# Kernel optimization log

Hardware: AMD Instinct MI355X
Metric: run time of the kernel (lower is better)

Reference implementation:

```python
import jax, jax.numpy as jnp
import numpy as np

N_ENTITY = 500000
N_RELATION = 1000
EMB = 128
BATCH = 131072


def setup_inputs() -> dict:
    key = jax.random.key(0)
    k_h, k_r, k_t, k_e, k_rel = jax.random.split(key, 5)
    head = jax.random.randint(k_h, (BATCH,), 0, N_ENTITY)
    rel = jax.random.randint(k_r, (BATCH,), 0, N_RELATION)
    tail = jax.random.randint(k_t, (BATCH,), 0, N_ENTITY)
    triple = jnp.stack([head, rel, tail], axis=1)  # [B,3] int
    # init_weights: uniform(-0.1, 0.1) for embeddings
    entity_emb = jax.random.uniform(k_e, (N_ENTITY, EMB), jnp.float32, -0.1, 0.1)
    relation_emb = jax.random.uniform(k_rel, (N_RELATION, EMB), jnp.float32, -0.1, 0.1)
    De = jnp.eye(EMB, dtype=jnp.float32)
    Dr = jnp.eye(EMB, dtype=jnp.float32)
    b_c = jnp.zeros((BATCH, EMB), dtype=jnp.float32)
    return {"triple": triple, "entity_emb": entity_emb, "relation_emb": relation_emb,
            "De": De, "Dr": Dr, "b_c": b_c}


def reference(triple, entity_emb, relation_emb, De, Dr, b_c):
    # flag == 0 path (default): combine head+relation, score against tail
    h = entity_emb[triple[:, 0]]        # [B,E] gather
    r = relation_emb[triple[:, 1]]      # [B,E] gather
    t = entity_emb[triple[:, 2]]        # [B,E] gather
    f = jnp.tanh(h @ De + r @ Dr + b_c)  # [B,E]
    score = jnp.sum(f * t, axis=1, keepdims=True)  # vectorized per-row dot -> [B,1]
    return jax.nn.sigmoid(score)
```

## Files before the change

kernel.cpp:

```cpp
#include <hip/hip_runtime.h>

#define EMB 128
#define BM 128
#define THREADS 512

typedef __attribute__((ext_vector_type(8))) short bf16x8;
typedef __attribute__((ext_vector_type(4))) float f32x4;
typedef unsigned short u16;

__device__ __forceinline__ u16 f2bf(float f) {
    unsigned u = __builtin_bit_cast(unsigned, f);
    u += 0x7fffu + ((u >> 16) & 1u);
    return (u16)(u >> 16);
}

__global__ void setup_kernel(const float* __restrict__ rel,
                             const float* __restrict__ Dr,
                             const float* __restrict__ De,
                             float* __restrict__ Rp,
                             u16* __restrict__ Bimg, int nrel) {
    const int blk = blockIdx.x;
    if (blk < 500) {
        const int n = threadIdx.x & 127;
        const int j = blk * 2 + (threadIdx.x >> 7);
        if (j >= nrel) return;
        float a = 0.f;
        for (int k = 0; k < EMB; ++k)
            a = fmaf(rel[(size_t)j * EMB + k], Dr[(size_t)k * EMB + n], a);
        Rp[(size_t)j * EMB + n] = a;
    } else {
        const int idx  = (blk - 500) * 256 + threadIdx.x;
        const int e    = idx & 7;
        const int lane = (idx >> 3) & 63;
        const int frag = idx >> 9;
        const int ni = frag & 7, kk = frag >> 3;
        const int k = kk * 32 + (lane >> 4) * 8 + e;
        const int n = ni * 16 + (lane & 15);
        Bimg[idx] = f2bf(De[(size_t)k * EMB + n]);
    }
}

__global__ __launch_bounds__(THREADS, 4)
void projE_main(const int* __restrict__ triple,
                const float* __restrict__ ent,
                const float* __restrict__ bc,
                const float* __restrict__ Rp,
                const u16* __restrict__ Bimg,
                float* __restrict__ out)
{
    __shared__ u16 As[BM][EMB];
    __shared__ u16 Bs[16384];

    const int tid  = threadIdx.x;
    const int lane = tid & 63;
    const int w    = tid >> 6;
    const int l15  = lane & 15;
    const int l4   = lane >> 4;
    const int bm0  = blockIdx.x * BM;

    {
        const __attribute__((address_space(1))) char* gB =
            (const __attribute__((address_space(1))) char*)Bimg;
        __attribute__((address_space(3))) char* lB =
            (__attribute__((address_space(3))) char*)Bs;
        #pragma unroll
        for (int i = 0; i < 4; ++i) {
            const int off = (i * THREADS + tid) * 16;
            __builtin_amdgcn_global_load_lds(
                (const __attribute__((address_space(1))) void*)(gB + off),
                (__attribute__((address_space(3))) void*)(lB + off), 16, 0, 0);
        }
    }

    {
        const int seg   = lane & 31;
        const int rhalf = lane >> 5;
        #pragma unroll
        for (int it = 0; it < 8; ++it) {
            const int row  = w * 16 + it * 2 + rhalf;
            const int g    = bm0 + row;
            const int hidx = triple[g * 3];
            const float4 hv = *reinterpret_cast<const float4*>(ent + (size_t)hidx * EMB + seg * 4);
            ushort4 hp = { f2bf(hv.x), f2bf(hv.y), f2bf(hv.z), f2bf(hv.w) };
            *reinterpret_cast<ushort4*>(&As[row][(seg * 4) ^ ((row & 7) << 3)]) = hp;
        }
    }

    __syncthreads();

    f32x4 acc[8];
    #pragma unroll
    for (int ci = 0; ci < 8; ++ci) acc[ci] = (f32x4){0.f, 0.f, 0.f, 0.f};

    const int arow = w * 16 + l15;
    const int asw  = (arow & 7) << 3;
    #pragma unroll
    for (int kk = 0; kk < 4; ++kk) {
        const bf16x8 h = *reinterpret_cast<const bf16x8*>(&As[arow][(kk * 32 + 8 * l4) ^ asw]);
        #pragma unroll
        for (int ci = 0; ci < 8; ++ci) {
            const bf16x8 d = *reinterpret_cast<const bf16x8*>(&Bs[(kk * 8 + ci) * 512 + lane * 8]);
            acc[ci] = __builtin_amdgcn_mfma_f32_16x16x32_bf16(d, h, acc[ci], 0, 0, 0);
        }
    }

    const int g    = bm0 + w * 16 + l15;
    const int ridx = triple[g * 3 + 1];
    const int tidx = triple[g * 3 + 2];
    const float* rp = Rp  + (size_t)ridx * EMB;
    const float* bp = bc  + (size_t)g    * EMB;
    const float* tp = ent + (size_t)tidx * EMB;

    float dot = 0.f;
    #pragma unroll
    for (int ci = 0; ci < 8; ++ci) {
        const int col = ci * 16 + 4 * l4;
        const float4 r4 = *reinterpret_cast<const float4*>(rp + col);
        const float4 b4 = *reinterpret_cast<const float4*>(bp + col);
        const float4 t4 = *reinterpret_cast<const float4*>(tp + col);
        #pragma unroll
        for (int e = 0; e < 4; ++e) {
            const float x  = acc[ci][e] + (&r4.x)[e] + (&b4.x)[e];
            const float e2 = __expf(2.f * x);
            const float fv = 1.f - __fdividef(2.f, e2 + 1.f);
            dot = fmaf(fv, (&t4.x)[e], dot);
        }
    }
    dot += __shfl_xor(dot, 16);
    dot += __shfl_xor(dot, 32);
    if (lane < 16) out[g] = __fdividef(1.f, 1.f + __expf(-dot));
}

extern "C" void kernel_launch(void* const* d_in, const int* in_sizes, int n_in,
                              void* d_out, int out_size, void* d_ws, size_t ws_size,
                              hipStream_t stream) {
    const int*   triple = (const int*)  d_in[0];
    const float* ent    = (const float*)d_in[1];
    const float* rel    = (const float*)d_in[2];
    const float* De     = (const float*)d_in[3];
    const float* Dr     = (const float*)d_in[4];
    const float* bc     = (const float*)d_in[5];
    float* out = (float*)d_out;

    const int batch = in_sizes[0] / 3;
    const int nrel  = in_sizes[2] / EMB;

    float* Rp = (float*)d_ws;
    u16* Bimg = (u16*)((char*)d_ws + 524288);

    setup_kernel<<<dim3(564), dim3(256), 0, stream>>>(rel, Dr, De, Rp, Bimg, nrel);
    projE_main<<<dim3(batch / BM), dim3(THREADS), 0, stream>>>(triple, ent, bc, Rp, Bimg, out);
}
```

Before: 46.04 us.

## Load head rows directly into MFMA fragments, drop LDS staging and barrier

```diff
diff --git a/kernel.cpp b/kernel.cpp
--- a/kernel.cpp
+++ b/kernel.cpp
@@ -48,9 +48,6 @@
                 const u16* __restrict__ Bimg,
                 float* __restrict__ out)
 {
-    __shared__ u16 As[BM][EMB];
-    __shared__ u16 Bs[16384];
-
     const int tid  = threadIdx.x;
     const int lane = tid & 63;
     const int w    = tid >> 6;
@@ -58,58 +55,57 @@
     const int l4   = lane >> 4;
     const int bm0  = blockIdx.x * BM;
 
-    {
-        const __attribute__((address_space(1))) char* gB =
-            (const __attribute__((address_space(1))) char*)Bimg;
-        __attribute__((address_space(3))) char* lB =
-            (__attribute__((address_space(3))) char*)Bs;
-        #pragma unroll
-        for (int i = 0; i < 4; ++i) {
-            const int off = (i * THREADS + tid) * 16;
-            __builtin_amdgcn_global_load_lds(
-                (const __attribute__((address_space(1))) void*)(gB + off),
-                (__attribute__((address_space(3))) void*)(lB + off), 16, 0, 0);
-        }
+    const int g    = bm0 + w * 16 + l15;
+    const int hidx = triple[g * 3 + 0];
+    const int ridx = triple[g * 3 + 1];
+    const int tidx = triple[g * 3 + 2];
+
+    const float* hp = ent + (size_t)hidx * EMB;
+    const float* tp = ent + (size_t)tidx * EMB;
+
+    float4 hv[8];
+    #pragma unroll
+    for (int kk = 0; kk < 4; ++kk) {
+        hv[2 * kk]     = *reinterpret_cast<const float4*>(hp + kk * 32 + 8 * l4);
+        hv[2 * kk + 1] = *reinterpret_cast<const float4*>(hp + kk * 32 + 8 * l4 + 4);
     }
 
-    {
-        const int seg   = lane & 31;
-        const int rhalf = lane >> 5;
-        #pragma unroll
-        for (int it = 0; it < 8; ++it) {
-            const int row  = w * 16 + it * 2 + rhalf;
-            const int g    = bm0 + row;
-            const int hidx = triple[g * 3];
-            const float4 hv = *reinterpret_cast<const float4*>(ent + (size_t)hidx * EMB + seg * 4);
-            ushort4 hp = { f2bf(hv.x), f2bf(hv.y), f2bf(hv.z), f2bf(hv.w) };
-            *reinterpret_cast<ushort4*>(&As[row][(seg * 4) ^ ((row & 7) << 3)]) = hp;
-        }
+    float4 tv[8];
+    #pragma unroll
+    for (int ci = 0; ci < 8; ++ci)
+        tv[ci] = *reinterpret_cast<const float4*>(tp + ci * 16 + 4 * l4);
+
+    bf16x8 hf[4];
+    #pragma unroll
+    for (int kk = 0; kk < 4; ++kk) {
+        bf16x8 v;
+        v[0] = (short)f2bf(hv[2 * kk].x);
+        v[1] = (short)f2bf(hv[2 * kk].y);
+        v[2] = (short)f2bf(hv[2 * kk].z);
+        v[3] = (short)f2bf(hv[2 * kk].w);
+        v[4] = (short)f2bf(hv[2 * kk + 1].x);
+        v[5] = (short)f2bf(hv[2 * kk + 1].y);
+        v[6] = (short)f2bf(hv[2 * kk + 1].z);
+        v[7] = (short)f2bf(hv[2 * kk + 1].w);
+        hf[kk] = v;
     }
-
-    __syncthreads();
 
     f32x4 acc[8];
     #pragma unroll
     for (int ci = 0; ci < 8; ++ci) acc[ci] = (f32x4){0.f, 0.f, 0.f, 0.f};
 
-    const int arow = w * 16 + l15;
-    const int asw  = (arow & 7) << 3;
     #pragma unroll
     for (int kk = 0; kk < 4; ++kk) {
-        const bf16x8 h = *reinterpret_cast<const bf16x8*>(&As[arow][(kk * 32 + 8 * l4) ^ asw]);
         #pragma unroll
         for (int ci = 0; ci < 8; ++ci) {
-            const bf16x8 d = *reinterpret_cast<const bf16x8*>(&Bs[(kk * 8 + ci) * 512 + lane * 8]);
-            acc[ci] = __builtin_amdgcn_mfma_f32_16x16x32_bf16(d, h, acc[ci], 0, 0, 0);
+            const bf16x8 d = *reinterpret_cast<const bf16x8*>(
+                Bimg + (((kk * 8 + ci) << 6) + lane) * 8);
+            acc[ci] = __builtin_amdgcn_mfma_f32_16x16x32_bf16(d, hf[kk], acc[ci], 0, 0, 0);
         }
     }
 
-    const int g    = bm0 + w * 16 + l15;
-    const int ridx = triple[g * 3 + 1];
-    const int tidx = triple[g * 3 + 2];
-    const float* rp = Rp  + (size_t)ridx * EMB;
-    const float* bp = bc  + (size_t)g    * EMB;
-    const float* tp = ent + (size_t)tidx * EMB;
+    const float* rp = Rp + (size_t)ridx * EMB;
+    const float* bp = bc + (size_t)g    * EMB;
 
     float dot = 0.f;
     #pragma unroll
@@ -117,13 +113,12 @@
         const int col = ci * 16 + 4 * l4;
         const float4 r4 = *reinterpret_cast<const float4*>(rp + col);
         const float4 b4 = *reinterpret_cast<const float4*>(bp + col);
-        const float4 t4 = *reinterpret_cast<const float4*>(tp + col);
         #pragma unroll
         for (int e = 0; e < 4; ++e) {
             const float x  = acc[ci][e] + (&r4.x)[e] + (&b4.x)[e];
             const float e2 = __expf(2.f * x);
             const float fv = 1.f - __fdividef(2.f, e2 + 1.f);
-            dot = fmaf(fv, (&t4.x)[e], dot);
+            dot = fmaf(fv, (&tv[ci].x)[e], dot);
         }
     }
     dot += __shfl_xor(dot, 16);
```

Measured after the change: 56.21 us. +22.1%, slower.
